# Optimization experiments

Measured on AMD Instinct MI355X. Metric: run time of the kernel, lower is better.

The kernel has to match this reference:

```python
import jax, jax.numpy as jnp
import numpy as np
from jax import lax

B, C_IN, C_OUT, L, K, PAD = 4, 16, 16, 1024, 5, 2


def setup_inputs() -> dict:
    key = jax.random.key(0)
    k1, k2 = jax.random.split(key)
    scores = jax.random.normal(k1, (B, C_IN, L, L), dtype=jnp.float32)
    # kaiming_uniform_(a=sqrt(5)) -> bound = 1/sqrt(fan_in), fan_in = (C_IN/groups)*K*K
    fan_in = C_IN * K * K
    bound = 1.0 / np.sqrt(fan_in)
    weight = jax.random.uniform(k2, (C_OUT, C_IN, K, K), dtype=jnp.float32,
                                minval=-bound, maxval=bound)
    bias = jnp.zeros((C_OUT,), dtype=jnp.float32)
    return {"scores": scores, "weight": weight, "bias": bias}


def reference(scores, weight, bias):
    # scores: [B, C_in, L, L]
    Lq = scores.shape[-2]
    causal = jnp.tril(jnp.ones((Lq, Lq), dtype=bool))  # [L, L]
    # mask_{-inf} then softmax over key dim
    masked = jnp.where(causal, scores, -jnp.inf)
    probs = jax.nn.softmax(masked, axis=-1)
    # grouped conv2d over the [L, L] score map (shape-preserving padding)
    out = lax.conv_general_dilated(
        probs, weight,
        window_strides=(1, 1),
        padding=((PAD, PAD), (PAD, PAD)),
        rhs_dilation=(1, 1),
        dimension_numbers=("NCHW", "OIHW", "NCHW"),
        feature_group_count=1,
    )
    out = out + bias[None, :, None, None]
    # mask_{0}: zero out non-causal positions
    out = jnp.where(causal, out, jnp.zeros((), dtype=out.dtype))
    return out
```

## Files before the change

### kernel.cpp

```cpp
#include <hip/hip_runtime.h>
#include <hip/hip_bf16.h>
#include <math.h>

#define LSEQ  1024
#define CIN   16
#define COUT  16
#define BATCH 4
#define TILE  16
#define NT    13
#define CSTR  48
#define RSTR  (20 * CSTR)

#define WFRAG_BYTES (NT * 64 * 8 * 2)
#define PROBS_ELEMS ((size_t)BATCH * CIN * LSEQ * LSEQ)
#define WS_NEEDED   (WFRAG_BYTES + PROBS_ELEMS * 2)

typedef __attribute__((ext_vector_type(8))) short short8;
typedef __attribute__((ext_vector_type(4))) float f32x4;
typedef __attribute__((ext_vector_type(4))) int   i32x4;

static __device__ __forceinline__ unsigned f2bf_u(float f) {
    unsigned u = __builtin_bit_cast(unsigned, f);
    return (u + 0x7fff + ((u >> 16) & 1)) >> 16;
}
static __device__ __forceinline__ unsigned short f2bf(float f) { return (unsigned short)f2bf_u(f); }

__global__ __launch_bounds__(256) void softmax_probs_kernel(
    const float* __restrict__ scores,
    const float* __restrict__ weight,
    ushort* __restrict__ wfrag,
    ushort* __restrict__ probs)
{
    const int tid = threadIdx.x;

    if (blockIdx.x == (BATCH * CIN * LSEQ / 4)) {
        for (int slot = tid; slot < NT * 64; slot += 256) {
            const int t = slot >> 6, lane = slot & 63;
            const int co = lane & 15, q = lane >> 4;
            const int ci0 = (q & 1) * 8, cb = q >> 1;
            const int c = 2 * t + cb;
            ushort* dst = wfrag + (size_t)slot * 8;
            #pragma unroll
            for (int jj = 0; jj < 8; ++jj) {
                float wv = (c < 25) ? weight[co * (CIN * 25) + (ci0 + jj) * 25 + c] : 0.f;
                dst[jj] = f2bf(wv);
            }
        }
        return;
    }

    const int w    = blockIdx.x * 4 + (tid >> 6);
    const int lane = tid & 63;
    const int i    = w & (LSEQ - 1);
    const float* rowp = scores + (size_t)w * LSEQ;

    float e[16];
    #pragma unroll
    for (int c = 0; c < 4; ++c) {
        const int j0 = c * 256 + lane * 4;
        float4 v = make_float4(0.f, 0.f, 0.f, 0.f);
        if (c * 256 <= i) v = *(const float4*)(rowp + j0);
        e[c*4+0] = (j0 + 0 <= i) ? __expf(v.x) : 0.f;
        e[c*4+1] = (j0 + 1 <= i) ? __expf(v.y) : 0.f;
        e[c*4+2] = (j0 + 2 <= i) ? __expf(v.z) : 0.f;
        e[c*4+3] = (j0 + 3 <= i) ? __expf(v.w) : 0.f;
    }
    float s = 0.f;
    #pragma unroll
    for (int t = 0; t < 16; ++t) s += e[t];
    #pragma unroll
    for (int off = 32; off > 0; off >>= 1) s += __shfl_xor(s, off, 64);
    const float rinv = 1.0f / s;

    ushort* prow = probs + (size_t)w * LSEQ;
    #pragma unroll
    for (int c = 0; c < 4; ++c) {
        if (c * 256 <= i) {
            const int j0 = c * 256 + lane * 4;
            uint2 pk;
            pk.x = f2bf_u(e[c*4+0] * rinv) | (f2bf_u(e[c*4+1] * rinv) << 16);
            pk.y = f2bf_u(e[c*4+2] * rinv) | (f2bf_u(e[c*4+3] * rinv) << 16);
            *(uint2*)(prow + j0) = pk;
        }
    }
}

__global__ __launch_bounds__(256) void conv_mfma2_kernel(
    const ushort* __restrict__ probs,
    const float* __restrict__ bias,
    const ushort* __restrict__ wfrag,
    float* __restrict__ out)
{
    const int jt = blockIdx.x, it = blockIdx.y, b = blockIdx.z;
    const int j0 = jt * TILE, i0 = it * TILE;
    const int tid = threadIdx.x;

    if (jt > it) {
        #pragma unroll
        for (int vv = 0; vv < 4; ++vv) {
            int e  = vv * 256 + tid;
            int co = e >> 6, il = (e >> 2) & 15, jq = e & 3;
            *(float4*)(out + ((size_t)(b * COUT + co) * LSEQ + i0 + il) * LSEQ + j0 + jq * 4)
                = make_float4(0.f, 0.f, 0.f, 0.f);
        }
        return;
    }

    const int lane = tid & 63;
    const int w    = tid >> 6;
    const int n    = lane & 15;
    const int q    = lane >> 4;

    short8 af[NT];
    #pragma unroll
    for (int t = 0; t < NT; ++t)
        af[t] = *(const short8*)(wfrag + (size_t)(t * 64 + lane) * 8);

    float bs[4];
    #pragma unroll
    for (int r = 0; r < 4; ++r) bs[r] = bias[q * 4 + r];

    int addr[NT];
    {
        const int cb  = q >> 1;
        const int cio = (q & 1) * 16;
        #pragma unroll
        for (int t = 0; t < NT; ++t) {
            int c = 2 * t + cb;
            if (c >= 25) addr[t] = 0;
            else {
                int kh = c / 5, kw = c - kh * 5;
                addr[t] = (kh * 20 + (n + kw)) * CSTR + cio + w * (4 * RSTR);
            }
        }
    }

    __shared__ ushort ptile[20 * 20 * 24];

    const ushort* pb = probs + (size_t)b * CIN * LSEQ * LSEQ;
    #pragma unroll
    for (int u = 0; u < 4; ++u) {
        const int e = u * 256 + tid;
        if (e < 800) {
            const int half = e & 1, cell = e >> 1;
            const int rr = cell / 20, cc = cell - rr * 20;
            const int row = i0 - 2 + rr;
            const int col = j0 - 2 + cc;
            const bool ok = (row >= 0) && (row < LSEQ) && (col >= 0) && (col < LSEQ) && (col <= row);
            const size_t base = ok ? ((size_t)row * LSEQ + col + (size_t)half * 8 * LSEQ * LSEQ) : 0;
            unsigned uu[8];
            #pragma unroll
            for (int k = 0; k < 8; ++k)
                uu[k] = pb[base + (size_t)k * LSEQ * LSEQ];
            i32x4 pk;
            #pragma unroll
            for (int k = 0; k < 4; ++k) {
                unsigned v = uu[2*k] | (uu[2*k+1] << 16);
                pk[k] = ok ? (int)v : 0;
            }
            *(i32x4*)((char*)ptile + cell * CSTR + half * 16) = pk;
        }
    }
    __syncthreads();

    #pragma unroll
    for (int s = 0; s < 4; ++s) {
        f32x4 acc = {0.f, 0.f, 0.f, 0.f};
        #pragma unroll
        for (int t = 0; t < NT; ++t) {
            short8 bf = *(const short8*)((const char*)ptile + addr[t] + s * RSTR);
            acc = __builtin_amdgcn_mfma_f32_16x16x32_bf16(af[t], bf, acc, 0, 0, 0);
        }
        const int i = i0 + w * 4 + s;
        const int j = j0 + n;
        #pragma unroll
        for (int r = 0; r < 4; ++r) {
            const int co = q * 4 + r;
            out[((size_t)(b * COUT + co) * LSEQ + i) * LSEQ + j] = (j <= i) ? (acc[r] + bs[r]) : 0.f;
        }
    }
}

__global__ __launch_bounds__(256) void stats_fb_kernel(const float* __restrict__ scores,
                                                       float* __restrict__ rowinv)
{
    const int w   = blockIdx.x;
    const int row = w & (LSEQ - 1);
    const int tid = threadIdx.x;
    const int j0  = tid * 4;
    float4 v = make_float4(0.f, 0.f, 0.f, 0.f);
    if (j0 <= row) v = *(const float4*)(scores + (size_t)w * LSEQ + j0);
    float s = 0.f;
    s += (j0 + 0 <= row) ? __expf(v.x) : 0.f;
    s += (j0 + 1 <= row) ? __expf(v.y) : 0.f;
    s += (j0 + 2 <= row) ? __expf(v.z) : 0.f;
    s += (j0 + 3 <= row) ? __expf(v.w) : 0.f;
    #pragma unroll
    for (int off = 32; off > 0; off >>= 1) s += __shfl_xor(s, off, 64);
    __shared__ float part[4];
    if ((tid & 63) == 0) part[tid >> 6] = s;
    __syncthreads();
    if (tid == 0) rowinv[w] = 1.0f / (part[0] + part[1] + part[2] + part[3]);
}

__global__ void wprep_fb_kernel(const float* __restrict__ weight, ushort* __restrict__ wfrag)
{
    const int lane = threadIdx.x;
    const int co   = lane & 15;
    const int q    = lane >> 4;
    const int ci0  = (q & 1) * 8;
    const int cb   = q >> 1;
    for (int t = 0; t < NT; ++t) {
        const int c = 2 * t + cb;
        ushort* dst = wfrag + (size_t)(t * 64 + lane) * 8;
        #pragma unroll
        for (int jj = 0; jj < 8; ++jj) {
            float wv = (c < 25) ? weight[co * (CIN * 25) + (ci0 + jj) * 25 + c] : 0.f;
            dst[jj] = f2bf(wv);
        }
    }
}

__global__ __launch_bounds__(256) void conv_fb_kernel(
    const float* __restrict__ scores,
    const float* __restrict__ bias,
    const float* __restrict__ rowinv,
    const ushort* __restrict__ wfrag,
    float* __restrict__ out)
{
    const int jt = blockIdx.x, it = blockIdx.y, b = blockIdx.z;
    const int j0 = jt * TILE, i0 = it * TILE;
    const int tid = threadIdx.x;

    if (jt > it) {
        #pragma unroll
        for (int vv = 0; vv < 4; ++vv) {
            int e  = vv * 256 + tid;
            int co = e >> 6, il = (e >> 2) & 15, jq = e & 3;
            *(float4*)(out + ((size_t)(b * COUT + co) * LSEQ + i0 + il) * LSEQ + j0 + jq * 4)
                = make_float4(0.f, 0.f, 0.f, 0.f);
        }
        return;
    }

    const int lane = tid & 63;
    const int w    = tid >> 6;
    const int n    = lane & 15;
    const int q    = lane >> 4;

    short8 af[NT];
    #pragma unroll
    for (int t = 0; t < NT; ++t)
        af[t] = *(const short8*)(wfrag + (size_t)(t * 64 + lane) * 8);

    float bs[4];
    #pragma unroll
    for (int r = 0; r < 4; ++r) bs[r] = bias[q * 4 + r];

    int addr[NT];
    {
        const int cb  = q >> 1;
        const int cio = (q & 1) * 16;
        #pragma unroll
        for (int t = 0; t < NT; ++t) {
            int c = 2 * t + cb;
            if (c >= 25) addr[t] = 0;
            else {
                int kh = c / 5, kw = c - kh * 5;
                addr[t] = (kh * 20 + (n + kw)) * CSTR + cio + w * (4 * RSTR);
            }
        }
    }

    __shared__ ushort ptile[20 * 20 * 24];

    for (int u = 0; u < 8; ++u) {
        int e = u * 256 + tid;
        if (e < 1920) {
            int ci  = e / 120;
            int rem = e - ci * 120;
            int rr  = rem / 6;
            int cq  = rem - rr * 6;
            int row  = i0 - 2 + rr;
            int gcol = j0 - 4 + cq * 4;
            bool rok = (row >= 0) && (row < LSEQ);
            float rinv = 0.f;
            float4 v = make_float4(0.f, 0.f, 0.f, 0.f);
            if (rok) {
                int rid = (b * CIN + ci) * LSEQ + row;
                rinv = rowinv[rid];
                if (gcol >= 0 && gcol <= LSEQ - 4 && gcol <= row)
                    v = *(const float4*)(scores + (size_t)rid * LSEQ + gcol);
            }
            float pv[4] = {v.x, v.y, v.z, v.w};
            #pragma unroll
            for (int l = 0; l < 4; ++l) {
                int col = gcol + l;
                int cc  = cq * 4 - 2 + l;
                bool ok = rok && col >= 0 && col < LSEQ && col <= row;
                float p = ok ? __expf(pv[l]) * rinv : 0.f;
                if (cc >= 0 && cc < 20)
                    ptile[(rr * 20 + cc) * 24 + ci] = f2bf(p);
            }
        }
    }
    __syncthreads();

    #pragma unroll
    for (int s = 0; s < 4; ++s) {
        f32x4 acc = {0.f, 0.f, 0.f, 0.f};
        #pragma unroll
        for (int t = 0; t < NT; ++t) {
            short8 bf = *(const short8*)((const char*)ptile + addr[t] + s * RSTR);
            acc = __builtin_amdgcn_mfma_f32_16x16x32_bf16(af[t], bf, acc, 0, 0, 0);
        }
        const int i = i0 + w * 4 + s;
        const int j = j0 + n;
        #pragma unroll
        for (int r = 0; r < 4; ++r) {
            const int co = q * 4 + r;
            out[((size_t)(b * COUT + co) * LSEQ + i) * LSEQ + j] = (j <= i) ? (acc[r] + bs[r]) : 0.f;
        }
    }
}

extern "C" void kernel_launch(void* const* d_in, const int* in_sizes, int n_in,
                              void* d_out, int out_size, void* d_ws, size_t ws_size,
                              hipStream_t stream) {
    const float* scores = (const float*)d_in[0];
    const float* weight = (const float*)d_in[1];
    const float* bias   = (const float*)d_in[2];
    float* out = (float*)d_out;

    if (ws_size >= WS_NEEDED) {
        ushort* wfrag = (ushort*)d_ws;
        ushort* probs = (ushort*)((char*)d_ws + WFRAG_BYTES);

        softmax_probs_kernel<<<BATCH * CIN * LSEQ / 4 + 1, 256, 0, stream>>>(
            scores, weight, wfrag, probs);

        dim3 g(LSEQ / TILE, LSEQ / TILE, BATCH);
        conv_mfma2_kernel<<<g, 256, 0, stream>>>(probs, bias, wfrag, out);
    } else {
        float*  rowinv = (float*)d_ws;
        ushort* wfrag  = (ushort*)((char*)d_ws + (size_t)BATCH * CIN * LSEQ * 4);

        stats_fb_kernel<<<BATCH * CIN * LSEQ, 256, 0, stream>>>(scores, rowinv);
        wprep_fb_kernel<<<1, 64, 0, stream>>>(weight, wfrag);

        dim3 g(LSEQ / TILE, LSEQ / TILE, BATCH);
        conv_fb_kernel<<<g, 256, 0, stream>>>(scores, bias, rowinv, wfrag, out);
    }
}
```

Before: 550.5 us.

## Store bf16 probs channel-interleaved so conv tile loads become 16-byte vector reads

The softmax kernel now gives each block one (batch,row) across all 16 channels. It stages the bf16 probabilities in shared memory and writes them in a [B,L,L,C] channel-last layout. The conv kernel then loads each 8-channel half-cell with a single 16-byte vector load instead of 8 strided 2-byte gathers. The cost is 32KB of shared memory per softmax block, an extra sync and a transpose pass, and fewer, larger softmax blocks.

```diff
diff --git a/kernel.cpp b/kernel.cpp
--- a/kernel.cpp
+++ b/kernel.cpp
@@ -33,7 +33,7 @@
 {
     const int tid = threadIdx.x;
 
-    if (blockIdx.x == (BATCH * CIN * LSEQ / 4)) {
+    if (blockIdx.x == BATCH * LSEQ) {
         for (int slot = tid; slot < NT * 64; slot += 256) {
             const int t = slot >> 6, lane = slot & 63;
             const int co = lane & 15, q = lane >> 4;
@@ -49,39 +49,64 @@
         return;
     }
 
-    const int w    = blockIdx.x * 4 + (tid >> 6);
+    __shared__ ushort sm[CIN * LSEQ];
+
+    const int bi   = blockIdx.x;
+    const int b    = bi >> 10;
+    const int row  = bi & (LSEQ - 1);
+    const int wv   = tid >> 6;
     const int lane = tid & 63;
-    const int i    = w & (LSEQ - 1);
-    const float* rowp = scores + (size_t)w * LSEQ;
-
-    float e[16];
-    #pragma unroll
-    for (int c = 0; c < 4; ++c) {
-        const int j0 = c * 256 + lane * 4;
-        float4 v = make_float4(0.f, 0.f, 0.f, 0.f);
-        if (c * 256 <= i) v = *(const float4*)(rowp + j0);
-        e[c*4+0] = (j0 + 0 <= i) ? __expf(v.x) : 0.f;
-        e[c*4+1] = (j0 + 1 <= i) ? __expf(v.y) : 0.f;
-        e[c*4+2] = (j0 + 2 <= i) ? __expf(v.z) : 0.f;
-        e[c*4+3] = (j0 + 3 <= i) ? __expf(v.w) : 0.f;
-    }
-    float s = 0.f;
-    #pragma unroll
-    for (int t = 0; t < 16; ++t) s += e[t];
-    #pragma unroll
-    for (int off = 32; off > 0; off >>= 1) s += __shfl_xor(s, off, 64);
-    const float rinv = 1.0f / s;
-
-    ushort* prow = probs + (size_t)w * LSEQ;
-    #pragma unroll
-    for (int c = 0; c < 4; ++c) {
-        if (c * 256 <= i) {
+
+    #pragma unroll
+    for (int m = 0; m < 4; ++m) {
+        const int ci = wv * 4 + m;
+        const float* rowp = scores + ((size_t)(b * CIN + ci) * LSEQ + row) * LSEQ;
+
+        float e[16];
+        #pragma unroll
+        for (int c = 0; c < 4; ++c) {
             const int j0 = c * 256 + lane * 4;
-            uint2 pk;
-            pk.x = f2bf_u(e[c*4+0] * rinv) | (f2bf_u(e[c*4+1] * rinv) << 16);
-            pk.y = f2bf_u(e[c*4+2] * rinv) | (f2bf_u(e[c*4+3] * rinv) << 16);
-            *(uint2*)(prow + j0) = pk;
-        }
+            float4 v = make_float4(0.f, 0.f, 0.f, 0.f);
+            if (c * 256 <= row) v = *(const float4*)(rowp + j0);
+            e[c*4+0] = (j0 + 0 <= row) ? __expf(v.x) : 0.f;
+            e[c*4+1] = (j0 + 1 <= row) ? __expf(v.y) : 0.f;
+            e[c*4+2] = (j0 + 2 <= row) ? __expf(v.z) : 0.f;
+            e[c*4+3] = (j0 + 3 <= row) ? __expf(v.w) : 0.f;
+        }
+        float s = 0.f;
+        #pragma unroll
+        for (int t = 0; t < 16; ++t) s += e[t];
+        #pragma unroll
+        for (int off = 32; off > 0; off >>= 1) s += __shfl_xor(s, off, 64);
+        const float rinv = 1.0f / s;
+
+        ushort* smrow = sm + ci * LSEQ;
+        #pragma unroll
+        for (int c = 0; c < 4; ++c) {
+            if (c * 256 <= row) {
+                const int j0 = c * 256 + lane * 4;
+                uint2 pk;
+                pk.x = f2bf_u(e[c*4+0] * rinv) | (f2bf_u(e[c*4+1] * rinv) << 16);
+                pk.y = f2bf_u(e[c*4+2] * rinv) | (f2bf_u(e[c*4+3] * rinv) << 16);
+                *(uint2*)(smrow + j0) = pk;
+            }
+        }
+    }
+    __syncthreads();
+
+    ushort* prow = probs + ((size_t)b * LSEQ + row) * (LSEQ * CIN);
+    const int nch = 2 * (row + 1);
+    for (int chunk = tid; chunk < nch; chunk += 256) {
+        const int col = chunk >> 1;
+        const int h   = chunk & 1;
+        i32x4 pk;
+        #pragma unroll
+        for (int k = 0; k < 4; ++k) {
+            unsigned lo = sm[(h * 8 + 2 * k    ) * LSEQ + col];
+            unsigned hi = sm[(h * 8 + 2 * k + 1) * LSEQ + col];
+            pk[k] = (int)(lo | (hi << 16));
+        }
+        *(i32x4*)(prow + (size_t)col * CIN + h * 8) = pk;
     }
 }
 
@@ -137,7 +162,7 @@
 
     __shared__ ushort ptile[20 * 20 * 24];
 
-    const ushort* pb = probs + (size_t)b * CIN * LSEQ * LSEQ;
+    const ushort* pb = probs + (size_t)b * (LSEQ * LSEQ * CIN);
     #pragma unroll
     for (int u = 0; u < 4; ++u) {
         const int e = u * 256 + tid;
@@ -147,17 +172,9 @@
             const int row = i0 - 2 + rr;
             const int col = j0 - 2 + cc;
             const bool ok = (row >= 0) && (row < LSEQ) && (col >= 0) && (col < LSEQ) && (col <= row);
-            const size_t base = ok ? ((size_t)row * LSEQ + col + (size_t)half * 8 * LSEQ * LSEQ) : 0;
-            unsigned uu[8];
-            #pragma unroll
-            for (int k = 0; k < 8; ++k)
-                uu[k] = pb[base + (size_t)k * LSEQ * LSEQ];
-            i32x4 pk;
-            #pragma unroll
-            for (int k = 0; k < 4; ++k) {
-                unsigned v = uu[2*k] | (uu[2*k+1] << 16);
-                pk[k] = ok ? (int)v : 0;
-            }
+            i32x4 pk = {0, 0, 0, 0};
+            if (ok)
+                pk = *(const i32x4*)(pb + ((size_t)row * LSEQ + col) * CIN + half * 8);
             *(i32x4*)((char*)ptile + cell * CSTR + half * 16) = pk;
         }
     }
@@ -336,7 +353,7 @@
         ushort* wfrag = (ushort*)d_ws;
         ushort* probs = (ushort*)((char*)d_ws + WFRAG_BYTES);
 
-        softmax_probs_kernel<<<BATCH * CIN * LSEQ / 4 + 1, 256, 0, stream>>>(
+        softmax_probs_kernel<<<BATCH * LSEQ + 1, 256, 0, stream>>>(
             scores, weight, wfrag, probs);
 
         dim3 g(LSEQ / TILE, LSEQ / TILE, BATCH);
```

New measurement: 521.2 us. -5.3%, faster.
